# Kernel tuning notes

Hardware: AMD Instinct MI355X
Metric: run time of the kernel (lower is better)

## Reference

```python
import jax, jax.numpy as jnp
import numpy as np

N = 200000   # nodes per branch
E = 600000   # directed edges per branch
G = 8192     # graphs per batch
F_IN = 7
H = 128
OUT = 2
BN_EPS = 1e-5


def setup_inputs() -> dict:
    key = jax.random.key(0)
    ks = jax.random.split(key, 16)
    s = 0.05
    inp = {
        "x_c": jax.random.normal(ks[0], (N, F_IN), jnp.float32),
        "edge_index_c": jax.random.randint(ks[1], (2, E), 0, N, jnp.int32),
        "batch_c": jnp.sort(jax.random.randint(ks[2], (N,), 0, G, jnp.int32)),
        "x_s": jax.random.normal(ks[3], (N, F_IN), jnp.float32),
        "edge_index_s": jax.random.randint(ks[4], (2, E), 0, N, jnp.int32),
        "batch_s": jnp.sort(jax.random.randint(ks[5], (N,), 0, G, jnp.int32)),
        "Wc0": jax.random.normal(ks[6], (F_IN, H), jnp.float32) * s,
        "bc0": jnp.zeros((H,), jnp.float32),
        "Wc1": jax.random.normal(ks[7], (H, H), jnp.float32) * s,
        "bc1": jnp.zeros((H,), jnp.float32),
        "bnc_gamma": jnp.ones((2, H), jnp.float32),
        "bnc_beta": jnp.zeros((2, H), jnp.float32),
        "bnc_mean": jax.random.normal(ks[8], (2, H), jnp.float32) * 0.01,
        "bnc_var": jnp.ones((2, H), jnp.float32),
        "Ws0": jax.random.normal(ks[9], (F_IN, H), jnp.float32) * s,
        "bs0": jnp.zeros((H,), jnp.float32),
        "Ws1": jax.random.normal(ks[10], (H, H), jnp.float32) * s,
        "bs1": jnp.zeros((H,), jnp.float32),
        "bns_gamma": jnp.ones((2, H), jnp.float32),
        "bns_beta": jnp.zeros((2, H), jnp.float32),
        "bns_mean": jax.random.normal(ks[11], (2, H), jnp.float32) * 0.01,
        "bns_var": jnp.ones((2, H), jnp.float32),
        "fc1_w": jax.random.normal(ks[12], (2 * H, H), jnp.float32) * s,
        "fc1_b": jnp.zeros((H,), jnp.float32),
        "fc2_w": jax.random.normal(ks[13], (H, OUT), jnp.float32) * s,
        "fc2_b": jnp.zeros((OUT,), jnp.float32),
        "num_graphs": G,
    }
    return inp


def _gcn_conv(x, src, dst, W, b):
    """PyG GCNConv: D^{-1/2}(A+I)D^{-1/2} X W + b, self-loops added."""
    n = x.shape[0]
    h = x @ W                                   # [n, H]
    loop = jnp.arange(n, dtype=src.dtype)
    src2 = jnp.concatenate([src, loop])
    dst2 = jnp.concatenate([dst, loop])
    deg = jax.ops.segment_sum(jnp.ones_like(dst2, h.dtype), dst2, num_segments=n)
    dinv = jnp.where(deg > 0, jax.lax.rsqrt(deg), 0.0)
    coef = (dinv[src2] * dinv[dst2])[:, None]   # [E+n, 1]
    out = jax.ops.segment_sum(h[src2] * coef, dst2, num_segments=n)
    return out + b


def _branch(x, ei, W0, b0, W1, b1, gamma, beta, mean, var):
    src, dst = ei[0], ei[1]
    for i, (W, b) in enumerate(((W0, b0), (W1, b1))):
        x = _gcn_conv(x, src, dst, W, b)
        # BatchNorm1d (eval mode) + ReLU; dropout is identity in eval
        x = (x - mean[i]) * jax.lax.rsqrt(var[i] + BN_EPS) * gamma[i] + beta[i]
        x = jax.nn.relu(x)
    return x


def _mean_pool(x, batch, num_graphs):
    s = jax.ops.segment_sum(x, batch, num_segments=num_graphs)
    cnt = jax.ops.segment_sum(jnp.ones_like(batch, x.dtype), batch, num_segments=num_graphs)
    return s / jnp.maximum(cnt, 1.0)[:, None]


def reference(x_c, edge_index_c, batch_c, x_s, edge_index_s, batch_s,
              Wc0, bc0, Wc1, bc1, bnc_gamma, bnc_beta, bnc_mean, bnc_var,
              Ws0, bs0, Ws1, bs1, bns_gamma, bns_beta, bns_mean, bns_var,
              fc1_w, fc1_b, fc2_w, fc2_b, num_graphs):
    hc = _branch(x_c, edge_index_c, Wc0, bc0, Wc1, bc1,
                 bnc_gamma, bnc_beta, bnc_mean, bnc_var)
    hs = _branch(x_s, edge_index_s, Ws0, bs0, Ws1, bs1,
                 bns_gamma, bns_beta, bns_mean, bns_var)
    pc = _mean_pool(hc, batch_c, num_graphs)   # [G, H]
    ps = _mean_pool(hs, batch_s, num_graphs)   # [G, H]
    x = jnp.concatenate([pc, ps], axis=1)      # [G, 2H]
    x = jax.nn.relu(x @ fc1_w + fc1_b)
    return x @ fc2_w + fc2_b                   # [G, 2]
```

## Files before the change

### kernel.cpp

```cpp
#include <hip/hip_runtime.h>

#define NN 200000
#define NE 600000
#define NG 8192
#define HD 128
#define FIN 7
#define BN_EPS 1e-5f

#define CHUNK 1024
#define NB 196
#define TA 64
#define NBT (NN / TA)
#define ECAP 320

__global__ void k_hist(const int* __restrict__ dstC, const int* __restrict__ dstS,
                       const int* __restrict__ batchC, const int* __restrict__ batchS,
                       int* __restrict__ degC, int* __restrict__ degS,
                       int* __restrict__ cntC, int* __restrict__ cntS) {
    int e = blockIdx.x * 256 + threadIdx.x;
    if (e < NE)            atomicAdd(&degC[dstC[e]], 1);
    else if (e < 2 * NE)   atomicAdd(&degS[dstS[e - NE]], 1);
    if (e < NN)                      atomicAdd(&cntC[batchC[e]], 1);
    else if (e >= NE && e < NE + NN) atomicAdd(&cntS[batchS[e - NE]], 1);
}

__global__ void k_scan1m(const int* __restrict__ degC, const int* __restrict__ degS,
                         int* __restrict__ bsumC, int* __restrict__ bsumS,
                         float* __restrict__ dinvC, float* __restrict__ dinvS,
                         const float* __restrict__ xC, const float* __restrict__ xS,
                         float* __restrict__ xsC, float* __restrict__ xsS) {
    __shared__ int sd[256];
    int t = threadIdx.x;
    int b = blockIdx.x;
    bool sBr = b >= NB;
    int bb = sBr ? b - NB : b;
    const int* deg = sBr ? degS : degC;
    const float* x = sBr ? xS : xC;
    float* dinv = sBr ? dinvS : dinvC;
    float* xs   = sBr ? xsS : xsC;
    int* bsum = sBr ? bsumS : bsumC;
    int base = bb * CHUNK + t * 4;
    int s = 0;
#pragma unroll
    for (int j = 0; j < 4; j++) {
        int i = base + j;
        if (i < NN) {
            int d = deg[i];
            s += d;
            float di = rsqrtf((float)(d + 1));
            dinv[i] = di;
            float4 v0, v1;
            v0.x = x[(size_t)i * FIN + 0] * di;
            v0.y = x[(size_t)i * FIN + 1] * di;
            v0.z = x[(size_t)i * FIN + 2] * di;
            v0.w = x[(size_t)i * FIN + 3] * di;
            v1.x = x[(size_t)i * FIN + 4] * di;
            v1.y = x[(size_t)i * FIN + 5] * di;
            v1.z = x[(size_t)i * FIN + 6] * di;
            v1.w = 0.f;
            *reinterpret_cast<float4*>(&xs[(size_t)i * 8])     = v0;
            *reinterpret_cast<float4*>(&xs[(size_t)i * 8 + 4]) = v1;
        }
    }
    sd[t] = s; __syncthreads();
    for (int st = 128; st > 0; st >>= 1) { if (t < st) sd[t] += sd[t + st]; __syncthreads(); }
    if (t == 0) bsum[bb] = sd[0];
}

__global__ void k_scan2m(int* __restrict__ bsumC, int* __restrict__ bsumS) {
    __shared__ int sd[256];
    int* bsum = blockIdx.x ? bsumS : bsumC;
    int t = threadIdx.x;
    int v = (t < NB) ? bsum[t] : 0;
    sd[t] = v; __syncthreads();
    for (int st = 1; st < 256; st <<= 1) {
        int add = (t >= st) ? sd[t - st] : 0;
        __syncthreads();
        sd[t] += add;
        __syncthreads();
    }
    if (t < NB) bsum[t] = sd[t] - v;
}

__global__ void k_scan3m(const int* __restrict__ degC, const int* __restrict__ degS,
                         const int* __restrict__ bsumC, const int* __restrict__ bsumS,
                         int* __restrict__ offsC, int* __restrict__ offsS,
                         int* __restrict__ curC, int* __restrict__ curS) {
    __shared__ int sd[256];
    int t = threadIdx.x;
    int b = blockIdx.x;
    bool sBr = b >= NB;
    int bb = sBr ? b - NB : b;
    const int* deg  = sBr ? degS  : degC;
    const int* bsum = sBr ? bsumS : bsumC;
    int* offs   = sBr ? offsS : offsC;
    int* cursor = sBr ? curS  : curC;
    int base = bb * CHUNK + t * 4;
    int v[4]; int s = 0;
#pragma unroll
    for (int j = 0; j < 4; j++) { int i = base + j; v[j] = (i < NN) ? deg[i] : 0; s += v[j]; }
    sd[t] = s; __syncthreads();
    for (int st = 1; st < 256; st <<= 1) {
        int add = (t >= st) ? sd[t - st] : 0;
        __syncthreads();
        sd[t] += add;
        __syncthreads();
    }
    int run = bsum[bb] + sd[t] - s;
#pragma unroll
    for (int j = 0; j < 4; j++) {
        int i = base + j;
        if (i < NN) { offs[i] = run; cursor[i] = run; run += v[j]; }
    }
    if (bb == 0 && t == 0) offs[NN] = NE;
}

__global__ void k_fillm(const int* __restrict__ srcC, const int* __restrict__ dstC,
                        const int* __restrict__ srcS, const int* __restrict__ dstS,
                        int* __restrict__ curC, int* __restrict__ curS,
                        int* __restrict__ csrC, int* __restrict__ csrS) {
    int e = blockIdx.x * 256 + threadIdx.x;
    if (e < NE) {
        int d = dstC[e];
        int pos = atomicAdd(&curC[d], 1);
        csrC[pos] = srcC[e];
    } else if (e < 2 * NE) {
        int ee = e - NE;
        int d = dstS[ee];
        int pos = atomicAdd(&curS[d], 1);
        csrS[pos] = srcS[ee];
    }
}

__global__ void k_aggxm(const float* __restrict__ xsC, const float* __restrict__ xsS,
                        const float* __restrict__ dinvC, const float* __restrict__ dinvS,
                        const int* __restrict__ offsC, const int* __restrict__ offsS,
                        const int* __restrict__ csrC, const int* __restrict__ csrS,
                        float* __restrict__ axdC, float* __restrict__ axdS) {
    int gid = blockIdx.x * 256 + threadIdx.x;
    bool sBr = gid >= NN * 8;
    int lid = sBr ? gid - NN * 8 : gid;
    const float* xs   = sBr ? xsS   : xsC;
    const float* dinv = sBr ? dinvS : dinvC;
    const int*   offs = sBr ? offsS : offsC;
    const int*   csr  = sBr ? csrS  : csrC;
    float*       axd  = sBr ? axdS  : axdC;
    int i = lid >> 3, f = lid & 7;
    float v = xs[lid];
    int o1 = offs[i], o2 = offs[i + 1];
    int j = o1;
    for (; j + 2 <= o2; j += 2) {
        int s0 = csr[j], s1 = csr[j + 1];
        float u0 = xs[(size_t)s0 * 8 + f];
        float u1 = xs[(size_t)s1 * 8 + f];
        v += u0; v += u1;
    }
    if (j < o2) v += xs[(size_t)csr[j] * 8 + f];
    float di = dinv[i];
    axd[lid] = (f == 7) ? di : v * di;
}

__device__ __forceinline__ void src_contrib(const float* __restrict__ axd, int s,
                                            const float4* wp, const float4 c4, float4& a) {
    float4 r0 = *reinterpret_cast<const float4*>(&axd[(size_t)s * 8]);
    float4 r1 = *reinterpret_cast<const float4*>(&axd[(size_t)s * 8 + 4]);
    float axr[7] = { r0.x, r0.y, r0.z, r0.w, r1.x, r1.y, r1.z };
    float4 y = c4;
#pragma unroll
    for (int k = 0; k < FIN; k++) {
        y.x = fmaf(axr[k], wp[k].x, y.x);
        y.y = fmaf(axr[k], wp[k].y, y.y);
        y.z = fmaf(axr[k], wp[k].z, y.z);
        y.w = fmaf(axr[k], wp[k].w, y.w);
    }
    a.x = fmaf(fmaxf(y.x, 0.f), r1.w, a.x);
    a.y = fmaf(fmaxf(y.y, 0.f), r1.w, a.y);
    a.z = fmaf(fmaxf(y.z, 0.f), r1.w, a.z);
    a.w = fmaf(fmaxf(y.w, 0.f), r1.w, a.w);
}

__global__ __launch_bounds__(256, 4) void k_agp2(
    const float* __restrict__ axdC, const float* __restrict__ axdS,
    const float* __restrict__ dinvC, const float* __restrict__ dinvS,
    const int* __restrict__ offsC, const int* __restrict__ offsS,
    const int* __restrict__ csrC, const int* __restrict__ csrS,
    const int* __restrict__ batchC, const int* __restrict__ batchS,
    const float* __restrict__ Wc0, const float* __restrict__ bc0,
    const float* __restrict__ bncG, const float* __restrict__ bncB,
    const float* __restrict__ bncM, const float* __restrict__ bncV,
    const float* __restrict__ Wc1, const float* __restrict__ bc1,
    const float* __restrict__ Ws0, const float* __restrict__ bs0,
    const float* __restrict__ bnsG, const float* __restrict__ bnsB,
    const float* __restrict__ bnsM, const float* __restrict__ bnsV,
    const float* __restrict__ Ws1, const float* __restrict__ bs1,
    float* __restrict__ poolC, float* __restrict__ poolS)
{
    __shared__ float g2[TA][132];
    __shared__ int soffs[TA + 1];
    __shared__ int scsr[ECAP];
    int b = blockIdx.x;
    bool sBr = b >= NBT;
    int bb = sBr ? b - NBT : b;
    const float* axd  = sBr ? axdS  : axdC;
    const float* dinv = sBr ? dinvS : dinvC;
    const int*  offs  = sBr ? offsS : offsC;
    const int*  csr   = sBr ? csrS  : csrC;
    const int*  batch = sBr ? batchS : batchC;
    const float* W0   = sBr ? Ws0 : Wc0;
    const float* b0   = sBr ? bs0 : bc0;
    const float* bnG  = sBr ? bnsG : bncG;
    const float* bnB  = sBr ? bnsB : bncB;
    const float* bnM  = sBr ? bnsM : bncM;
    const float* bnV  = sBr ? bnsV : bncV;
    const float* W1   = sBr ? Ws1 : Wc1;
    const float* b1   = sBr ? bs1 : bc1;
    float* pool       = sBr ? poolS : poolC;

    int t = threadIdx.x;
    int nbase = bb * TA;
    if (t <= TA) soffs[t] = offs[nbase + t];
    __syncthreads();
    int E0 = soffs[0], E1 = soffs[TA];
    int ecap = (E1 - E0) < ECAP ? (E1 - E0) : ECAP;
    for (int j = t; j < ecap; j += 256) scsr[j] = csr[E0 + j];

    int q = t & 31, ng = t >> 5;
    int f4 = q * 4, n0 = ng * 8;

    float4 gm = *reinterpret_cast<const float4*>(&bnG[f4]);
    float4 vr = *reinterpret_cast<const float4*>(&bnV[f4]);
    float4 mn = *reinterpret_cast<const float4*>(&bnM[f4]);
    float4 bt = *reinterpret_cast<const float4*>(&bnB[f4]);
    float4 bb0 = *reinterpret_cast<const float4*>(&b0[f4]);
    float4 gsc;
    gsc.x = gm.x * rsqrtf(vr.x + BN_EPS);
    gsc.y = gm.y * rsqrtf(vr.y + BN_EPS);
    gsc.z = gm.z * rsqrtf(vr.z + BN_EPS);
    gsc.w = gm.w * rsqrtf(vr.w + BN_EPS);
    float4 wp[FIN];
#pragma unroll
    for (int k = 0; k < FIN; k++) {
        float4 w = *reinterpret_cast<const float4*>(&W0[k * HD + f4]);
        wp[k] = make_float4(w.x * gsc.x, w.y * gsc.y, w.z * gsc.z, w.w * gsc.w);
    }
    float4 c4 = make_float4((bb0.x - mn.x) * gsc.x + bt.x,
                            (bb0.y - mn.y) * gsc.y + bt.y,
                            (bb0.z - mn.z) * gsc.z + bt.z,
                            (bb0.w - mn.w) * gsc.w + bt.w);
    __syncthreads();

#pragma unroll
    for (int n = 0; n < 8; n++) {
        int ln = n0 + n;
        float4 a = make_float4(0.f, 0.f, 0.f, 0.f);
        src_contrib(axd, nbase + ln, wp, c4, a);
        int e = soffs[ln], ee = soffs[ln + 1];
        for (; e < ee; e++) {
            int j = e - E0;
            int s = (j < ECAP) ? scsr[j] : csr[e];
            src_contrib(axd, s, wp, c4, a);
        }
        *reinterpret_cast<float4*>(&g2[ln][f4]) = a;
    }
    __syncthreads();

    float acc[8][4];
#pragma unroll
    for (int a = 0; a < 8; a++)
#pragma unroll
        for (int c = 0; c < 4; c++) acc[a][c] = 0.f;

    for (int k = 0; k < 128; k += 4) {
        float ha[8][4];
#pragma unroll
        for (int a = 0; a < 8; a++) {
            float4 hv = *reinterpret_cast<const float4*>(&g2[n0 + a][k]);
            ha[a][0] = hv.x; ha[a][1] = hv.y; ha[a][2] = hv.z; ha[a][3] = hv.w;
        }
#pragma unroll
        for (int j = 0; j < 4; j++) {
            float4 w = *reinterpret_cast<const float4*>(&W1[(k + j) * HD + f4]);
#pragma unroll
            for (int a = 0; a < 8; a++) {
                acc[a][0] = fmaf(ha[a][j], w.x, acc[a][0]);
                acc[a][1] = fmaf(ha[a][j], w.y, acc[a][1]);
                acc[a][2] = fmaf(ha[a][j], w.z, acc[a][2]);
                acc[a][3] = fmaf(ha[a][j], w.w, acc[a][3]);
            }
        }
    }

    float4 gm2 = *reinterpret_cast<const float4*>(&bnG[HD + f4]);
    float4 bt2 = *reinterpret_cast<const float4*>(&bnB[HD + f4]);
    float4 mn2 = *reinterpret_cast<const float4*>(&bnM[HD + f4]);
    float4 vr2 = *reinterpret_cast<const float4*>(&bnV[HD + f4]);
    float4 bb1 = *reinterpret_cast<const float4*>(&b1[f4]);
    float Ax = gm2.x * rsqrtf(vr2.x + BN_EPS), Bx = (bb1.x - mn2.x) * Ax + bt2.x;
    float Ay = gm2.y * rsqrtf(vr2.y + BN_EPS), By = (bb1.y - mn2.y) * Ay + bt2.y;
    float Az = gm2.z * rsqrtf(vr2.z + BN_EPS), Bz = (bb1.z - mn2.z) * Az + bt2.z;
    float Aw = gm2.w * rsqrtf(vr2.w + BN_EPS), Bw = (bb1.w - mn2.w) * Aw + bt2.w;

    float sx = 0, sy = 0, sz = 0, sw = 0;
    int curg = -1;
#pragma unroll
    for (int a = 0; a < 8; a++) {
        int i = nbase + n0 + a;
        int g = batch[i];
        float sdv = dinv[i];
        float zx = fmaxf(fmaf(acc[a][0] * sdv, Ax, Bx), 0.f);
        float zy = fmaxf(fmaf(acc[a][1] * sdv, Ay, By), 0.f);
        float zz = fmaxf(fmaf(acc[a][2] * sdv, Az, Bz), 0.f);
        float zw = fmaxf(fmaf(acc[a][3] * sdv, Aw, Bw), 0.f);
        if (g != curg) {
            if (curg >= 0) {
                atomicAdd(&pool[curg * HD + f4 + 0], sx);
                atomicAdd(&pool[curg * HD + f4 + 1], sy);
                atomicAdd(&pool[curg * HD + f4 + 2], sz);
                atomicAdd(&pool[curg * HD + f4 + 3], sw);
            }
            curg = g; sx = zx; sy = zy; sz = zz; sw = zw;
        } else { sx += zx; sy += zy; sz += zz; sw += zw; }
    }
    atomicAdd(&pool[curg * HD + f4 + 0], sx);
    atomicAdd(&pool[curg * HD + f4 + 1], sy);
    atomicAdd(&pool[curg * HD + f4 + 2], sz);
    atomicAdd(&pool[curg * HD + f4 + 3], sw);
}

#define GPB 16
__global__ __launch_bounds__(128) void k_mlp(
    const float* __restrict__ pc, const float* __restrict__ ps,
    const int* __restrict__ cc, const int* __restrict__ cs,
    const float* __restrict__ w1, const float* __restrict__ b1,
    const float* __restrict__ w2, const float* __restrict__ b2,
    float* __restrict__ outp)
{
    __shared__ float xc[GPB][256];
    __shared__ float hb[GPB][128];
    int t = threadIdx.x;
    int g0 = blockIdx.x * GPB;
#pragma unroll
    for (int gg = 0; gg < GPB; gg++) {
        int g = g0 + gg;
        xc[gg][t]       = pc[g * HD + t] / fmaxf((float)cc[g], 1.f);
        xc[gg][128 + t] = ps[g * HD + t] / fmaxf((float)cs[g], 1.f);
    }
    __syncthreads();
    float acc[GPB];
#pragma unroll
    for (int gg = 0; gg < GPB; gg++) acc[gg] = b1[t];
#pragma unroll 2
    for (int k = 0; k < 256; k++) {
        float w = w1[k * HD + t];
#pragma unroll
        for (int gg = 0; gg < GPB; gg++) acc[gg] = fmaf(xc[gg][k], w, acc[gg]);
    }
#pragma unroll
    for (int gg = 0; gg < GPB; gg++) hb[gg][t] = fmaxf(acc[gg], 0.f);
    __syncthreads();
    if (t < GPB * 2) {
        int gg = t >> 1, o = t & 1;
        float v = b2[o];
        for (int k = 0; k < 128; k++) v = fmaf(hb[gg][k], w2[k * 2 + o], v);
        outp[(size_t)(g0 + gg) * 2 + o] = v;
    }
}

extern "C" void kernel_launch(void* const* d_in, const int* in_sizes, int n_in,
                              void* d_out, int out_size, void* d_ws, size_t ws_size,
                              hipStream_t stream) {
    const float* x_c      = (const float*)d_in[0];
    const int*   ei_c     = (const int*)  d_in[1];
    const int*   batch_c  = (const int*)  d_in[2];
    const float* x_s      = (const float*)d_in[3];
    const int*   ei_s     = (const int*)  d_in[4];
    const int*   batch_s  = (const int*)  d_in[5];
    const float* Wc0      = (const float*)d_in[6];
    const float* bc0      = (const float*)d_in[7];
    const float* Wc1      = (const float*)d_in[8];
    const float* bc1      = (const float*)d_in[9];
    const float* bnc_g    = (const float*)d_in[10];
    const float* bnc_b    = (const float*)d_in[11];
    const float* bnc_m    = (const float*)d_in[12];
    const float* bnc_v    = (const float*)d_in[13];
    const float* Ws0      = (const float*)d_in[14];
    const float* bs0      = (const float*)d_in[15];
    const float* Ws1      = (const float*)d_in[16];
    const float* bs1      = (const float*)d_in[17];
    const float* bns_g    = (const float*)d_in[18];
    const float* bns_b    = (const float*)d_in[19];
    const float* bns_m    = (const float*)d_in[20];
    const float* bns_v    = (const float*)d_in[21];
    const float* fc1_w    = (const float*)d_in[22];
    const float* fc1_b    = (const float*)d_in[23];
    const float* fc2_w    = (const float*)d_in[24];
    const float* fc2_b    = (const float*)d_in[25];

    char* p = (char*)d_ws;
    auto take = [&](size_t bytes) {
        void* r = (void*)p;
        p += (bytes + 255) & ~(size_t)255;
        return r;
    };
    float* xs_c   = (float*)take((size_t)NN * 8 * 4);
    float* xs_s   = (float*)take((size_t)NN * 8 * 4);
    float* axd_c  = (float*)take((size_t)NN * 8 * 4);
    float* axd_s  = (float*)take((size_t)NN * 8 * 4);
    int*   deg_c  = (int*)  take((size_t)NN * 4);
    int*   deg_s  = (int*)  take((size_t)NN * 4);
    float* dinv_c = (float*)take((size_t)NN * 4);
    float* dinv_s = (float*)take((size_t)NN * 4);
    int*   offs_c = (int*)  take((size_t)(NN + 1) * 4);
    int*   offs_s = (int*)  take((size_t)(NN + 1) * 4);
    int*   cur_c  = (int*)  take((size_t)NN * 4);
    int*   cur_s  = (int*)  take((size_t)NN * 4);
    int*   csr_c  = (int*)  take((size_t)NE * 4);
    int*   csr_s  = (int*)  take((size_t)NE * 4);
    int*   bsum_c = (int*)  take((size_t)NB * 4);
    int*   bsum_s = (int*)  take((size_t)NB * 4);
    float* pool_c = (float*)take((size_t)NG * HD * 4);
    float* pool_s = (float*)take((size_t)NG * HD * 4);
    int*   cnt_c  = (int*)  take((size_t)NG * 4);
    int*   cnt_s  = (int*)  take((size_t)NG * 4);
    (void)ws_size; (void)in_sizes; (void)n_in; (void)out_size;

    hipMemsetAsync(deg_c, 0, (size_t)2 * NN * 4, stream);
    hipMemsetAsync(pool_c, 0, ((size_t)2 * NG * HD + 2 * NG) * 4, stream);

    const int* src_c = ei_c;           const int* dst_c = ei_c + NE;
    const int* src_s = ei_s;           const int* dst_s = ei_s + NE;

    k_hist  <<<(2 * NE + 255) / 256, 256, 0, stream>>>(dst_c, dst_s, batch_c, batch_s,
                                                       deg_c, deg_s, cnt_c, cnt_s);
    k_scan1m<<<2 * NB, 256, 0, stream>>>(deg_c, deg_s, bsum_c, bsum_s, dinv_c, dinv_s,
                                         x_c, x_s, xs_c, xs_s);
    k_scan2m<<<2, 256, 0, stream>>>(bsum_c, bsum_s);
    k_scan3m<<<2 * NB, 256, 0, stream>>>(deg_c, deg_s, bsum_c, bsum_s,
                                         offs_c, offs_s, cur_c, cur_s);
    k_fillm <<<(2 * NE + 255) / 256, 256, 0, stream>>>(src_c, dst_c, src_s, dst_s,
                                                       cur_c, cur_s, csr_c, csr_s);
    k_aggxm <<<2 * NN * 8 / 256, 256, 0, stream>>>(xs_c, xs_s, dinv_c, dinv_s,
                                                   offs_c, offs_s, csr_c, csr_s, axd_c, axd_s);

    k_agp2<<<2 * NBT, 256, 0, stream>>>(axd_c, axd_s, dinv_c, dinv_s,
                                        offs_c, offs_s, csr_c, csr_s, batch_c, batch_s,
                                        Wc0, bc0, bnc_g, bnc_b, bnc_m, bnc_v, Wc1, bc1,
                                        Ws0, bs0, bns_g, bns_b, bns_m, bns_v, Ws1, bs1,
                                        pool_c, pool_s);

    k_mlp<<<NG / GPB, 128, 0, stream>>>(pool_c, pool_s, cnt_c, cnt_s,
                                        fc1_w, fc1_b, fc2_w, fc2_b, (float*)d_out);
}
```

Measured before the change: 528.3 us.

## Fuse first-layer aggregation into CSR fill via atomics, shrink node tiles

Removes the separate first-layer aggregation kernel. The CSR fill kernel now scatter-adds the scaled source features into a per-node sum buffer with float atomics, and the buffer is seeded with the self term and the node's inverse-sqrt degree. The fused layer kernel reads that sum (including the degree factor) directly, which drops the separate dinv array. Node tile size drops from 64 to 32 per block, launch bounds move to allow 8 blocks per CU, and the MLP processes 4 graphs per block instead of 16. The trade is a separate gather pass against 7 float atomics per edge with contention, plus nondeterministic summation order.

```diff
diff --git a/kernel.cpp b/kernel.cpp
--- a/kernel.cpp
+++ b/kernel.cpp
@@ -9,9 +9,9 @@
 
 #define CHUNK 1024
 #define NB 196
-#define TA 64
+#define TA 32
 #define NBT (NN / TA)
-#define ECAP 320
+#define ECAP 224
 
 __global__ void k_hist(const int* __restrict__ dstC, const int* __restrict__ dstS,
                        const int* __restrict__ batchC, const int* __restrict__ batchS,
@@ -26,9 +26,9 @@
 
 __global__ void k_scan1m(const int* __restrict__ degC, const int* __restrict__ degS,
                          int* __restrict__ bsumC, int* __restrict__ bsumS,
-                         float* __restrict__ dinvC, float* __restrict__ dinvS,
                          const float* __restrict__ xC, const float* __restrict__ xS,
-                         float* __restrict__ xsC, float* __restrict__ xsS) {
+                         float* __restrict__ xsC, float* __restrict__ xsS,
+                         float* __restrict__ sumC, float* __restrict__ sumS) {
     __shared__ int sd[256];
     int t = threadIdx.x;
     int b = blockIdx.x;
@@ -36,8 +36,8 @@
     int bb = sBr ? b - NB : b;
     const int* deg = sBr ? degS : degC;
     const float* x = sBr ? xS : xC;
-    float* dinv = sBr ? dinvS : dinvC;
-    float* xs   = sBr ? xsS : xsC;
+    float* xs  = sBr ? xsS : xsC;
+    float* sum = sBr ? sumS : sumC;
     int* bsum = sBr ? bsumS : bsumC;
     int base = bb * CHUNK + t * 4;
     int s = 0;
@@ -48,7 +48,6 @@
             int d = deg[i];
             s += d;
             float di = rsqrtf((float)(d + 1));
-            dinv[i] = di;
             float4 v0, v1;
             v0.x = x[(size_t)i * FIN + 0] * di;
             v0.y = x[(size_t)i * FIN + 1] * di;
@@ -60,6 +59,9 @@
             v1.w = 0.f;
             *reinterpret_cast<float4*>(&xs[(size_t)i * 8])     = v0;
             *reinterpret_cast<float4*>(&xs[(size_t)i * 8 + 4]) = v1;
+            v1.w = di;
+            *reinterpret_cast<float4*>(&sum[(size_t)i * 8])     = v0;
+            *reinterpret_cast<float4*>(&sum[(size_t)i * 8 + 4]) = v1;
         }
     }
     sd[t] = s; __syncthreads();
@@ -118,70 +120,56 @@
 __global__ void k_fillm(const int* __restrict__ srcC, const int* __restrict__ dstC,
                         const int* __restrict__ srcS, const int* __restrict__ dstS,
                         int* __restrict__ curC, int* __restrict__ curS,
-                        int* __restrict__ csrC, int* __restrict__ csrS) {
+                        int* __restrict__ csrC, int* __restrict__ csrS,
+                        const float* __restrict__ xsC, const float* __restrict__ xsS,
+                        float* __restrict__ sumC, float* __restrict__ sumS) {
     int e = blockIdx.x * 256 + threadIdx.x;
-    if (e < NE) {
-        int d = dstC[e];
-        int pos = atomicAdd(&curC[d], 1);
-        csrC[pos] = srcC[e];
-    } else if (e < 2 * NE) {
-        int ee = e - NE;
-        int d = dstS[ee];
-        int pos = atomicAdd(&curS[d], 1);
-        csrS[pos] = srcS[ee];
-    }
-}
-
-__global__ void k_aggxm(const float* __restrict__ xsC, const float* __restrict__ xsS,
-                        const float* __restrict__ dinvC, const float* __restrict__ dinvS,
-                        const int* __restrict__ offsC, const int* __restrict__ offsS,
-                        const int* __restrict__ csrC, const int* __restrict__ csrS,
-                        float* __restrict__ axdC, float* __restrict__ axdS) {
-    int gid = blockIdx.x * 256 + threadIdx.x;
-    bool sBr = gid >= NN * 8;
-    int lid = sBr ? gid - NN * 8 : gid;
-    const float* xs   = sBr ? xsS   : xsC;
-    const float* dinv = sBr ? dinvS : dinvC;
-    const int*   offs = sBr ? offsS : offsC;
-    const int*   csr  = sBr ? csrS  : csrC;
-    float*       axd  = sBr ? axdS  : axdC;
-    int i = lid >> 3, f = lid & 7;
-    float v = xs[lid];
-    int o1 = offs[i], o2 = offs[i + 1];
-    int j = o1;
-    for (; j + 2 <= o2; j += 2) {
-        int s0 = csr[j], s1 = csr[j + 1];
-        float u0 = xs[(size_t)s0 * 8 + f];
-        float u1 = xs[(size_t)s1 * 8 + f];
-        v += u0; v += u1;
-    }
-    if (j < o2) v += xs[(size_t)csr[j] * 8 + f];
-    float di = dinv[i];
-    axd[lid] = (f == 7) ? di : v * di;
-}
-
-__device__ __forceinline__ void src_contrib(const float* __restrict__ axd, int s,
+    bool sBr = e >= NE;
+    if (e >= 2 * NE) return;
+    int ee = sBr ? e - NE : e;
+    const int* srcA = sBr ? srcS : srcC;
+    const int* dstA = sBr ? dstS : dstC;
+    int* cur = sBr ? curS : curC;
+    int* csr = sBr ? csrS : csrC;
+    const float* xs = sBr ? xsS : xsC;
+    float* sum = sBr ? sumS : sumC;
+    int s = srcA[ee], d = dstA[ee];
+    int pos = atomicAdd(&cur[d], 1);
+    csr[pos] = s;
+    float4 v0 = *reinterpret_cast<const float4*>(&xs[(size_t)s * 8]);
+    float4 v1 = *reinterpret_cast<const float4*>(&xs[(size_t)s * 8 + 4]);
+    float* dp = &sum[(size_t)d * 8];
+    atomicAdd(&dp[0], v0.x); atomicAdd(&dp[1], v0.y);
+    atomicAdd(&dp[2], v0.z); atomicAdd(&dp[3], v0.w);
+    atomicAdd(&dp[4], v1.x); atomicAdd(&dp[5], v1.y);
+    atomicAdd(&dp[6], v1.z);
+}
+
+__device__ __forceinline__ void src_contrib(float4 r0, float4 r1,
                                             const float4* wp, const float4 c4, float4& a) {
-    float4 r0 = *reinterpret_cast<const float4*>(&axd[(size_t)s * 8]);
-    float4 r1 = *reinterpret_cast<const float4*>(&axd[(size_t)s * 8 + 4]);
     float axr[7] = { r0.x, r0.y, r0.z, r0.w, r1.x, r1.y, r1.z };
-    float4 y = c4;
+    float ds = r1.w;
+    float4 tt = make_float4(0.f, 0.f, 0.f, 0.f);
 #pragma unroll
     for (int k = 0; k < FIN; k++) {
-        y.x = fmaf(axr[k], wp[k].x, y.x);
-        y.y = fmaf(axr[k], wp[k].y, y.y);
-        y.z = fmaf(axr[k], wp[k].z, y.z);
-        y.w = fmaf(axr[k], wp[k].w, y.w);
-    }
-    a.x = fmaf(fmaxf(y.x, 0.f), r1.w, a.x);
-    a.y = fmaf(fmaxf(y.y, 0.f), r1.w, a.y);
-    a.z = fmaf(fmaxf(y.z, 0.f), r1.w, a.z);
-    a.w = fmaf(fmaxf(y.w, 0.f), r1.w, a.w);
-}
-
-__global__ __launch_bounds__(256, 4) void k_agp2(
-    const float* __restrict__ axdC, const float* __restrict__ axdS,
-    const float* __restrict__ dinvC, const float* __restrict__ dinvS,
+        tt.x = fmaf(axr[k], wp[k].x, tt.x);
+        tt.y = fmaf(axr[k], wp[k].y, tt.y);
+        tt.z = fmaf(axr[k], wp[k].z, tt.z);
+        tt.w = fmaf(axr[k], wp[k].w, tt.w);
+    }
+    float4 y;
+    y.x = fmaf(ds, tt.x, c4.x);
+    y.y = fmaf(ds, tt.y, c4.y);
+    y.z = fmaf(ds, tt.z, c4.z);
+    y.w = fmaf(ds, tt.w, c4.w);
+    a.x = fmaf(fmaxf(y.x, 0.f), ds, a.x);
+    a.y = fmaf(fmaxf(y.y, 0.f), ds, a.y);
+    a.z = fmaf(fmaxf(y.z, 0.f), ds, a.z);
+    a.w = fmaf(fmaxf(y.w, 0.f), ds, a.w);
+}
+
+__global__ __launch_bounds__(256, 8) void k_agp2(
+    const float* __restrict__ sumC, const float* __restrict__ sumS,
     const int* __restrict__ offsC, const int* __restrict__ offsS,
     const int* __restrict__ csrC, const int* __restrict__ csrS,
     const int* __restrict__ batchC, const int* __restrict__ batchS,
@@ -201,8 +189,7 @@
     int b = blockIdx.x;
     bool sBr = b >= NBT;
     int bb = sBr ? b - NBT : b;
-    const float* axd  = sBr ? axdS  : axdC;
-    const float* dinv = sBr ? dinvS : dinvC;
+    const float* sum  = sBr ? sumS  : sumC;
     const int*  offs  = sBr ? offsS : offsC;
     const int*  csr   = sBr ? csrS  : csrC;
     const int*  batch = sBr ? batchS : batchC;
@@ -225,7 +212,7 @@
     for (int j = t; j < ecap; j += 256) scsr[j] = csr[E0 + j];
 
     int q = t & 31, ng = t >> 5;
-    int f4 = q * 4, n0 = ng * 8;
+    int f4 = q * 4, n0 = ng * 4;
 
     float4 gm = *reinterpret_cast<const float4*>(&bnG[f4]);
     float4 vr = *reinterpret_cast<const float4*>(&bnV[f4]);
@@ -249,31 +236,39 @@
                             (bb0.w - mn.w) * gsc.w + bt.w);
     __syncthreads();
 
-#pragma unroll
-    for (int n = 0; n < 8; n++) {
+    float sdv4[4];
+#pragma unroll
+    for (int n = 0; n < 4; n++) {
         int ln = n0 + n;
         float4 a = make_float4(0.f, 0.f, 0.f, 0.f);
-        src_contrib(axd, nbase + ln, wp, c4, a);
+        {
+            float4 r0 = *reinterpret_cast<const float4*>(&sum[(size_t)(nbase + ln) * 8]);
+            float4 r1 = *reinterpret_cast<const float4*>(&sum[(size_t)(nbase + ln) * 8 + 4]);
+            sdv4[n] = r1.w;
+            src_contrib(r0, r1, wp, c4, a);
+        }
         int e = soffs[ln], ee = soffs[ln + 1];
         for (; e < ee; e++) {
             int j = e - E0;
             int s = (j < ECAP) ? scsr[j] : csr[e];
-            src_contrib(axd, s, wp, c4, a);
+            float4 r0 = *reinterpret_cast<const float4*>(&sum[(size_t)s * 8]);
+            float4 r1 = *reinterpret_cast<const float4*>(&sum[(size_t)s * 8 + 4]);
+            src_contrib(r0, r1, wp, c4, a);
         }
         *reinterpret_cast<float4*>(&g2[ln][f4]) = a;
     }
     __syncthreads();
 
-    float acc[8][4];
-#pragma unroll
-    for (int a = 0; a < 8; a++)
+    float acc[4][4];
+#pragma unroll
+    for (int a = 0; a < 4; a++)
 #pragma unroll
         for (int c = 0; c < 4; c++) acc[a][c] = 0.f;
 
     for (int k = 0; k < 128; k += 4) {
-        float ha[8][4];
-#pragma unroll
-        for (int a = 0; a < 8; a++) {
+        float ha[4][4];
+#pragma unroll
+        for (int a = 0; a < 4; a++) {
             float4 hv = *reinterpret_cast<const float4*>(&g2[n0 + a][k]);
             ha[a][0] = hv.x; ha[a][1] = hv.y; ha[a][2] = hv.z; ha[a][3] = hv.w;
         }
@@ -281,7 +276,7 @@
         for (int j = 0; j < 4; j++) {
             float4 w = *reinterpret_cast<const float4*>(&W1[(k + j) * HD + f4]);
 #pragma unroll
-            for (int a = 0; a < 8; a++) {
+            for (int a = 0; a < 4; a++) {
                 acc[a][0] = fmaf(ha[a][j], w.x, acc[a][0]);
                 acc[a][1] = fmaf(ha[a][j], w.y, acc[a][1]);
                 acc[a][2] = fmaf(ha[a][j], w.z, acc[a][2]);
@@ -303,10 +298,10 @@
     float sx = 0, sy = 0, sz = 0, sw = 0;
     int curg = -1;
 #pragma unroll
-    for (int a = 0; a < 8; a++) {
+    for (int a = 0; a < 4; a++) {
         int i = nbase + n0 + a;
         int g = batch[i];
-        float sdv = dinv[i];
+        float sdv = sdv4[a];
         float zx = fmaxf(fmaf(acc[a][0] * sdv, Ax, Bx), 0.f);
         float zy = fmaxf(fmaf(acc[a][1] * sdv, Ay, By), 0.f);
         float zz = fmaxf(fmaf(acc[a][2] * sdv, Az, Bz), 0.f);
@@ -327,7 +322,7 @@
     atomicAdd(&pool[curg * HD + f4 + 3], sw);
 }
 
-#define GPB 16
+#define GPB 4
 __global__ __launch_bounds__(128) void k_mlp(
     const float* __restrict__ pc, const float* __restrict__ ps,
     const int* __restrict__ cc, const int* __restrict__ cs,
@@ -349,7 +344,7 @@
     float acc[GPB];
 #pragma unroll
     for (int gg = 0; gg < GPB; gg++) acc[gg] = b1[t];
-#pragma unroll 2
+#pragma unroll 4
     for (int k = 0; k < 256; k++) {
         float w = w1[k * HD + t];
 #pragma unroll
@@ -404,12 +399,10 @@
     };
     float* xs_c   = (float*)take((size_t)NN * 8 * 4);
     float* xs_s   = (float*)take((size_t)NN * 8 * 4);
-    float* axd_c  = (float*)take((size_t)NN * 8 * 4);
-    float* axd_s  = (float*)take((size_t)NN * 8 * 4);
+    float* sum_c  = (float*)take((size_t)NN * 8 * 4);
+    float* sum_s  = (float*)take((size_t)NN * 8 * 4);
     int*   deg_c  = (int*)  take((size_t)NN * 4);
     int*   deg_s  = (int*)  take((size_t)NN * 4);
-    float* dinv_c = (float*)take((size_t)NN * 4);
-    float* dinv_s = (float*)take((size_t)NN * 4);
     int*   offs_c = (int*)  take((size_t)(NN + 1) * 4);
     int*   offs_s = (int*)  take((size_t)(NN + 1) * 4);
     int*   cur_c  = (int*)  take((size_t)NN * 4);
@@ -432,17 +425,16 @@
 
     k_hist  <<<(2 * NE + 255) / 256, 256, 0, stream>>>(dst_c, dst_s, batch_c, batch_s,
                                                        deg_c, deg_s, cnt_c, cnt_s);
-    k_scan1m<<<2 * NB, 256, 0, stream>>>(deg_c, deg_s, bsum_c, bsum_s, dinv_c, dinv_s,
-                                         x_c, x_s, xs_c, xs_s);
+    k_scan1m<<<2 * NB, 256, 0, stream>>>(deg_c, deg_s, bsum_c, bsum_s,
+                                         x_c, x_s, xs_c, xs_s, sum_c, sum_s);
     k_scan2m<<<2, 256, 0, stream>>>(bsum_c, bsum_s);
     k_scan3m<<<2 * NB, 256, 0, stream>>>(deg_c, deg_s, bsum_c, bsum_s,
                                          offs_c, offs_s, cur_c, cur_s);
     k_fillm <<<(2 * NE + 255) / 256, 256, 0, stream>>>(src_c, dst_c, src_s, dst_s,
-                                                       cur_c, cur_s, csr_c, csr_s);
-    k_aggxm <<<2 * NN * 8 / 256, 256, 0, stream>>>(xs_c, xs_s, dinv_c, dinv_s,
-                                                   offs_c, offs_s, csr_c, csr_s, axd_c, axd_s);
-
-    k_agp2<<<2 * NBT, 256, 0, stream>>>(axd_c, axd_s, dinv_c, dinv_s,
+                                                       cur_c, cur_s, csr_c, csr_s,
+                                                       xs_c, xs_s, sum_c, sum_s);
+
+    k_agp2<<<2 * NBT, 256, 0, stream>>>(sum_c, sum_s,
                                         offs_c, offs_s, csr_c, csr_s, batch_c, batch_s,
                                         Wc0, bc0, bnc_g, bnc_b, bnc_m, bnc_v, Wc1, bc1,
                                         Ws0, bs0, bns_g, bns_b, bns_m, bns_v, Ws1, bs1,
```

After: 1.036 ms. 96.2% more time.

## Pre-reduce mean pooling in shared memory and reuse loaded self-node dinv

Applied to the files above, without the earlier changes.

The fused GCN kernel now sums each block's per-graph pooled contributions into a shared-memory buffer of up to eight graph slots, then flushes them to global memory with one pass of atomics per block, replacing many per-thread global atomics. Each node's dinv is taken from the axd row already loaded for its self contribution instead of a separate global read. The g2 tile padding is removed, which may bring back shared-memory bank conflicts, and the extra shared buffer can lower occupancy. The MLP kernel handles fewer graphs per block with more unrolling, giving more blocks.

```diff
diff --git a/kernel.cpp b/kernel.cpp
--- a/kernel.cpp
+++ b/kernel.cpp
@@ -12,6 +12,7 @@
 #define TA 64
 #define NBT (NN / TA)
 #define ECAP 320
+#define GMAX 8
 
 __global__ void k_hist(const int* __restrict__ dstC, const int* __restrict__ dstS,
                        const int* __restrict__ batchC, const int* __restrict__ batchS,
@@ -160,10 +161,8 @@
     axd[lid] = (f == 7) ? di : v * di;
 }
 
-__device__ __forceinline__ void src_contrib(const float* __restrict__ axd, int s,
+__device__ __forceinline__ void src_contrib(float4 r0, float4 r1,
                                             const float4* wp, const float4 c4, float4& a) {
-    float4 r0 = *reinterpret_cast<const float4*>(&axd[(size_t)s * 8]);
-    float4 r1 = *reinterpret_cast<const float4*>(&axd[(size_t)s * 8 + 4]);
     float axr[7] = { r0.x, r0.y, r0.z, r0.w, r1.x, r1.y, r1.z };
     float4 y = c4;
 #pragma unroll
@@ -181,7 +180,6 @@
 
 __global__ __launch_bounds__(256, 4) void k_agp2(
     const float* __restrict__ axdC, const float* __restrict__ axdS,
-    const float* __restrict__ dinvC, const float* __restrict__ dinvS,
     const int* __restrict__ offsC, const int* __restrict__ offsS,
     const int* __restrict__ csrC, const int* __restrict__ csrS,
     const int* __restrict__ batchC, const int* __restrict__ batchS,
@@ -195,14 +193,14 @@
     const float* __restrict__ Ws1, const float* __restrict__ bs1,
     float* __restrict__ poolC, float* __restrict__ poolS)
 {
-    __shared__ float g2[TA][132];
+    __shared__ float g2[TA][HD];
+    __shared__ float spool[GMAX * HD];
     __shared__ int soffs[TA + 1];
     __shared__ int scsr[ECAP];
     int b = blockIdx.x;
     bool sBr = b >= NBT;
     int bb = sBr ? b - NBT : b;
     const float* axd  = sBr ? axdS  : axdC;
-    const float* dinv = sBr ? dinvS : dinvC;
     const int*  offs  = sBr ? offsS : offsC;
     const int*  csr   = sBr ? csrS  : csrC;
     const int*  batch = sBr ? batchS : batchC;
@@ -219,6 +217,8 @@
     int t = threadIdx.x;
     int nbase = bb * TA;
     if (t <= TA) soffs[t] = offs[nbase + t];
+#pragma unroll
+    for (int r = 0; r < GMAX * HD / 256; r++) spool[r * 256 + t] = 0.f;
     __syncthreads();
     int E0 = soffs[0], E1 = soffs[TA];
     int ecap = (E1 - E0) < ECAP ? (E1 - E0) : ECAP;
@@ -249,16 +249,24 @@
                             (bb0.w - mn.w) * gsc.w + bt.w);
     __syncthreads();
 
+    float sdv8[8];
 #pragma unroll
     for (int n = 0; n < 8; n++) {
         int ln = n0 + n;
         float4 a = make_float4(0.f, 0.f, 0.f, 0.f);
-        src_contrib(axd, nbase + ln, wp, c4, a);
+        {
+            float4 r0 = *reinterpret_cast<const float4*>(&axd[(size_t)(nbase + ln) * 8]);
+            float4 r1 = *reinterpret_cast<const float4*>(&axd[(size_t)(nbase + ln) * 8 + 4]);
+            sdv8[n] = r1.w;
+            src_contrib(r0, r1, wp, c4, a);
+        }
         int e = soffs[ln], ee = soffs[ln + 1];
         for (; e < ee; e++) {
             int j = e - E0;
             int s = (j < ECAP) ? scsr[j] : csr[e];
-            src_contrib(axd, s, wp, c4, a);
+            float4 r0 = *reinterpret_cast<const float4*>(&axd[(size_t)s * 8]);
+            float4 r1 = *reinterpret_cast<const float4*>(&axd[(size_t)s * 8 + 4]);
+            src_contrib(r0, r1, wp, c4, a);
         }
         *reinterpret_cast<float4*>(&g2[ln][f4]) = a;
     }
@@ -300,34 +308,61 @@
     float Az = gm2.z * rsqrtf(vr2.z + BN_EPS), Bz = (bb1.z - mn2.z) * Az + bt2.z;
     float Aw = gm2.w * rsqrtf(vr2.w + BN_EPS), Bw = (bb1.w - mn2.w) * Aw + bt2.w;
 
+    int gfirst = batch[nbase];
     float sx = 0, sy = 0, sz = 0, sw = 0;
     int curg = -1;
 #pragma unroll
     for (int a = 0; a < 8; a++) {
         int i = nbase + n0 + a;
         int g = batch[i];
-        float sdv = dinv[i];
+        float sdv = sdv8[a];
         float zx = fmaxf(fmaf(acc[a][0] * sdv, Ax, Bx), 0.f);
         float zy = fmaxf(fmaf(acc[a][1] * sdv, Ay, By), 0.f);
         float zz = fmaxf(fmaf(acc[a][2] * sdv, Az, Bz), 0.f);
         float zw = fmaxf(fmaf(acc[a][3] * sdv, Aw, Bw), 0.f);
         if (g != curg) {
             if (curg >= 0) {
-                atomicAdd(&pool[curg * HD + f4 + 0], sx);
-                atomicAdd(&pool[curg * HD + f4 + 1], sy);
-                atomicAdd(&pool[curg * HD + f4 + 2], sz);
-                atomicAdd(&pool[curg * HD + f4 + 3], sw);
+                int slot = curg - gfirst;
+                if (slot < GMAX) {
+                    atomicAdd(&spool[slot * HD + f4 + 0], sx);
+                    atomicAdd(&spool[slot * HD + f4 + 1], sy);
+                    atomicAdd(&spool[slot * HD + f4 + 2], sz);
+                    atomicAdd(&spool[slot * HD + f4 + 3], sw);
+                } else {
+                    atomicAdd(&pool[(size_t)curg * HD + f4 + 0], sx);
+                    atomicAdd(&pool[(size_t)curg * HD + f4 + 1], sy);
+                    atomicAdd(&pool[(size_t)curg * HD + f4 + 2], sz);
+                    atomicAdd(&pool[(size_t)curg * HD + f4 + 3], sw);
+                }
             }
             curg = g; sx = zx; sy = zy; sz = zz; sw = zw;
         } else { sx += zx; sy += zy; sz += zz; sw += zw; }
     }
-    atomicAdd(&pool[curg * HD + f4 + 0], sx);
-    atomicAdd(&pool[curg * HD + f4 + 1], sy);
-    atomicAdd(&pool[curg * HD + f4 + 2], sz);
-    atomicAdd(&pool[curg * HD + f4 + 3], sw);
-}
-
-#define GPB 16
+    {
+        int slot = curg - gfirst;
+        if (slot < GMAX) {
+            atomicAdd(&spool[slot * HD + f4 + 0], sx);
+            atomicAdd(&spool[slot * HD + f4 + 1], sy);
+            atomicAdd(&spool[slot * HD + f4 + 2], sz);
+            atomicAdd(&spool[slot * HD + f4 + 3], sw);
+        } else {
+            atomicAdd(&pool[(size_t)curg * HD + f4 + 0], sx);
+            atomicAdd(&pool[(size_t)curg * HD + f4 + 1], sy);
+            atomicAdd(&pool[(size_t)curg * HD + f4 + 2], sz);
+            atomicAdd(&pool[(size_t)curg * HD + f4 + 3], sw);
+        }
+    }
+    __syncthreads();
+
+    int glast = batch[nbase + TA - 1];
+    int nslots = glast - gfirst + 1;
+    if (nslots > GMAX) nslots = GMAX;
+    for (int idx = t; idx < (nslots << 7); idx += 256) {
+        atomicAdd(&pool[(size_t)(gfirst + (idx >> 7)) * HD + (idx & 127)], spool[idx]);
+    }
+}
+
+#define GPB 4
 __global__ __launch_bounds__(128) void k_mlp(
     const float* __restrict__ pc, const float* __restrict__ ps,
     const int* __restrict__ cc, const int* __restrict__ cs,
@@ -349,7 +384,7 @@
     float acc[GPB];
 #pragma unroll
     for (int gg = 0; gg < GPB; gg++) acc[gg] = b1[t];
-#pragma unroll 2
+#pragma unroll 4
     for (int k = 0; k < 256; k++) {
         float w = w1[k * HD + t];
 #pragma unroll
@@ -442,7 +477,7 @@
     k_aggxm <<<2 * NN * 8 / 256, 256, 0, stream>>>(xs_c, xs_s, dinv_c, dinv_s,
                                                    offs_c, offs_s, csr_c, csr_s, axd_c, axd_s);
 
-    k_agp2<<<2 * NBT, 256, 0, stream>>>(axd_c, axd_s, dinv_c, dinv_s,
+    k_agp2<<<2 * NBT, 256, 0, stream>>>(axd_c, axd_s,
                                         offs_c, offs_s, csr_c, csr_s, batch_c, batch_s,
                                         Wc0, bc0, bnc_g, bnc_b, bnc_m, bnc_v, Wc1, bc1,
                                         Ws0, bs0, bns_g, bns_b, bns_m, bns_v, Ws1, bs1,
```

Result: faster. 511.1 us (-3.2%).
